# Performance work log

Measured on AMD Instinct MI355X. Metric: run time of the kernel, lower is better.

Reference implementation:

```python
import jax, jax.numpy as jnp
import numpy as np

N_NODES = 50000
N_EDGES = 800000
D_FEAT = 64


def setup_inputs() -> dict:
    key = jax.random.key(0)
    kx, ks, kd = jax.random.split(key, 3)
    x = jax.random.normal(kx, (N_NODES, D_FEAT), dtype=jnp.float32)
    src = jax.random.randint(ks, (N_EDGES,), 0, N_NODES, dtype=jnp.int64)
    dst = jax.random.randint(kd, (N_EDGES,), 0, N_NODES, dtype=jnp.int64)
    return {"x": x, "src": src, "dst": dst}


def reference(x, src, dst):
    # SGC propagation: h[v] = sum_{(u->v) in E} x[u] / sqrt(out_deg(u) * out_deg(v))
    n = x.shape[0]
    # out-degrees: count of outgoing edges per node (matches graph.out_degrees())
    deg = jax.ops.segment_sum(jnp.ones(src.shape, x.dtype), src, num_segments=n)
    # per-edge normalization coefficient 1/sqrt(deg_u * deg_v)  [E]
    norm = 1.0 / jnp.sqrt(deg[src] * deg[dst])
    # gather-multiply-scatter-sum (u_mul_e_sum): messages flow src -> dst
    h = jax.ops.segment_sum(x[src] * norm[:, None], dst, num_segments=n)
    return h
```

## Files before the change

### kernel.cpp

```cpp
#include <hip/hip_runtime.h>

#define N_NODES 50000
#define N_EDGES 800000
#define D_FEAT 64

#define NBINS 2048
#define BSORT 100
#define SORT_CHUNK (N_EDGES / BSORT)
#define NSCAN (NBINS * BSORT)
#define SCAN_BLOCK 1024
#define SCAN_BLOCKS (NSCAN / SCAN_BLOCK)
#define AGG_CAP 4096
#define NAGG ((N_NODES + 31) / 32)

#define HCHUNKS 64
#define HCHUNK (N_EDGES / HCHUNKS)
#define HWORDS ((N_NODES + 3) / 4)

#define RS_BLOCKS ((N_NODES + 255) / 256)

__global__ __launch_bounds__(512)
void hist_count_kernel(const int* __restrict__ src, const int* __restrict__ dst,
                       unsigned int* __restrict__ hp32, unsigned int* __restrict__ gh) {
    __shared__ unsigned int lh[HWORDS];
    const int b = blockIdx.x, t = threadIdx.x;
    if (b < HCHUNKS) {
        for (int i = t; i < HWORDS; i += 512) lh[i] = 0u;
        __syncthreads();
        const int4* s4 = (const int4*)(src + b * HCHUNK);
        for (int i = t; i < HCHUNK / 4; i += 512) {
            int4 v = s4[i];
            atomicAdd(&lh[v.x >> 2], 1u << ((v.x & 3) * 8));
            atomicAdd(&lh[v.y >> 2], 1u << ((v.y & 3) * 8));
            atomicAdd(&lh[v.z >> 2], 1u << ((v.z & 3) * 8));
            atomicAdd(&lh[v.w >> 2], 1u << ((v.w & 3) * 8));
        }
        __syncthreads();
        for (int w = t; w < HWORDS; w += 512)
            hp32[(size_t)b * HWORDS + w] = lh[w];
    } else {
        const int cb = b - HCHUNKS;
        for (int i = t; i < NBINS; i += 512) lh[i] = 0;
        __syncthreads();
        const int4* d4 = (const int4*)(dst + cb * SORT_CHUNK);
        for (int i = t; i < SORT_CHUNK / 4; i += 512) {
            int4 v = d4[i];
            atomicAdd(&lh[v.x >> 5], 1u);
            atomicAdd(&lh[v.y >> 5], 1u);
            atomicAdd(&lh[v.z >> 5], 1u);
            atomicAdd(&lh[v.w >> 5], 1u);
        }
        __syncthreads();
        for (int i = t; i < NBINS; i += 512) gh[(size_t)i * BSORT + cb] = lh[i];
    }
}

__global__ __launch_bounds__(SCAN_BLOCK)
void scanred_rs_kernel(const unsigned int* __restrict__ gh, unsigned int* __restrict__ partial,
                       const unsigned char* __restrict__ hp8, float* __restrict__ rs) {
    const int b = blockIdx.x;
    if (b < SCAN_BLOCKS) {
        __shared__ unsigned int wsum[SCAN_BLOCK / 64];
        int g = b * SCAN_BLOCK + threadIdx.x;
        unsigned int v = gh[g];
        for (int off = 32; off > 0; off >>= 1) v += __shfl_down(v, off, 64);
        if ((threadIdx.x & 63) == 0) wsum[threadIdx.x >> 6] = v;
        __syncthreads();
        if (threadIdx.x < SCAN_BLOCK / 64) {
            unsigned int s = wsum[threadIdx.x];
            for (int off = SCAN_BLOCK / 128; off > 0; off >>= 1) s += __shfl_down(s, off, 64);
            if (threadIdx.x == 0) partial[b] = s;
        }
    } else {
        if (threadIdx.x < 256) {
            int v = (b - SCAN_BLOCKS) * 256 + threadIdx.x;
            if (v < N_NODES) {
                unsigned int s = 0;
                #pragma unroll
                for (int c = 0; c < HCHUNKS; ++c) s += hp8[(size_t)c * (HWORDS * 4) + v];
                rs[v] = rsqrtf((float)s);
            }
        }
    }
}

__global__ __launch_bounds__(SCAN_BLOCK)
void scan_final_kernel(unsigned int* __restrict__ data, const unsigned int* __restrict__ partial) {
    __shared__ unsigned int arr[SCAN_BLOCK];
    __shared__ unsigned int pbase[256];
    const int t = threadIdx.x;
    const int g = blockIdx.x * SCAN_BLOCK + t;
    if (t < 256) pbase[t] = (t < SCAN_BLOCKS) ? partial[t] : 0u;
    __syncthreads();
    for (int off = 1; off < 256; off <<= 1) {
        unsigned int u = (t < 256 && t >= off) ? pbase[t - off] : 0u;
        __syncthreads();
        if (t < 256 && t >= off) pbase[t] += u;
        __syncthreads();
    }
    const unsigned int base = (blockIdx.x == 0) ? 0u : pbase[blockIdx.x - 1];
    unsigned int v = data[g];
    arr[t] = v;
    __syncthreads();
    for (int off = 1; off < SCAN_BLOCK; off <<= 1) {
        unsigned int u = (t >= off) ? arr[t - off] : 0u;
        __syncthreads();
        arr[t] += u;
        __syncthreads();
    }
    data[g] = base + arr[t] - v;
}

__global__ __launch_bounds__(1024)
void bucket_scatter_kernel(const int* __restrict__ src, const int* __restrict__ dst,
                           const unsigned int* __restrict__ gh, unsigned int* __restrict__ keysB) {
    __shared__ unsigned int cur[NBINS];
    const int b = blockIdx.x, t = threadIdx.x;
    for (int i = t; i < NBINS; i += 1024) cur[i] = gh[(size_t)i * BSORT + b];
    __syncthreads();
    const int4* s4 = (const int4*)(src + b * SORT_CHUNK);
    const int4* d4 = (const int4*)(dst + b * SORT_CHUNK);
    for (int i = t; i < SORT_CHUNK / 4; i += 1024) {
        int4 s = s4[i];
        int4 d = d4[i];
        unsigned int p0 = atomicAdd(&cur[d.x >> 5], 1u);
        keysB[p0] = ((unsigned int)d.x << 16) | (unsigned int)s.x;
        unsigned int p1 = atomicAdd(&cur[d.y >> 5], 1u);
        keysB[p1] = ((unsigned int)d.y << 16) | (unsigned int)s.y;
        unsigned int p2 = atomicAdd(&cur[d.z >> 5], 1u);
        keysB[p2] = ((unsigned int)d.z << 16) | (unsigned int)s.z;
        unsigned int p3 = atomicAdd(&cur[d.w >> 5], 1u);
        keysB[p3] = ((unsigned int)d.w << 16) | (unsigned int)s.w;
    }
}

__global__ __launch_bounds__(512)
void bucket_aggregate_kernel(const float* __restrict__ x, const unsigned int* __restrict__ gh,
                             const unsigned int* __restrict__ keysB, const float* __restrict__ rs,
                             float* __restrict__ h) {
    __shared__ unsigned int ebuf[AGG_CAP];
    __shared__ unsigned int ecnt[32];
    __shared__ unsigned int eoff[33];
    const int g = blockIdx.x;
    const int t = threadIdx.x;
    const int lane = t & 63;
    const int w = t >> 6;
    const unsigned int base = gh[(size_t)g * BSORT];
    const unsigned int end  = gh[(size_t)(g + 1) * BSORT];
    const int cnt = (int)(end - base);

    if (cnt > 0 && cnt <= AGG_CAP) {
        if (t < 32) ecnt[t] = 0;
        __syncthreads();
        for (int i = t; i < cnt; i += 512) atomicAdd(&ecnt[(keysB[base + i] >> 16) & 31], 1u);
        __syncthreads();
        if (t == 0) {
            unsigned int r = 0;
            for (int k2 = 0; k2 < 32; ++k2) { eoff[k2] = r; r += ecnt[k2]; }
            eoff[32] = r;
        }
        __syncthreads();
        if (t < 32) ecnt[t] = eoff[t];
        __syncthreads();
        for (int i = t; i < cnt; i += 512) {
            unsigned int k = keysB[base + i];
            ebuf[atomicAdd(&ecnt[(k >> 16) & 31], 1u)] = k;
        }
        __syncthreads();

        const int grp = lane >> 4;
        const int fl  = lane & 15;
        for (int nl = w; nl < 32; nl += 8) {
            int node = g * 32 + nl;
            if (node >= N_NODES) continue;
            const int jb = (int)eoff[nl];
            const int m  = (int)eoff[nl + 1] - jb;
            float ax = 0.0f, ay = 0.0f, az = 0.0f, aw = 0.0f;
            int jj = 0;
            for (; jj + 8 <= m; jj += 8) {
                unsigned int s0 = ebuf[jb + jj + grp] & 0xFFFFu;
                unsigned int s1 = ebuf[jb + jj + 4 + grp] & 0xFFFFu;
                const float4 v0 = *(const float4*)&x[(size_t)s0 * D_FEAT + fl * 4];
                const float4 v1 = *(const float4*)&x[(size_t)s1 * D_FEAT + fl * 4];
                float w0 = rs[s0], w1 = rs[s1];
                ax = fmaf(v0.x, w0, ax); ay = fmaf(v0.y, w0, ay);
                az = fmaf(v0.z, w0, az); aw = fmaf(v0.w, w0, aw);
                ax = fmaf(v1.x, w1, ax); ay = fmaf(v1.y, w1, ay);
                az = fmaf(v1.z, w1, az); aw = fmaf(v1.w, w1, aw);
            }
            if (jj < m) {
                int idx = jj + grp;
                unsigned int s = ebuf[jb + min(idx, m - 1)] & 0xFFFFu;
                float wgt = (idx < m) ? rs[s] : 0.0f;
                const float4 v = *(const float4*)&x[(size_t)s * D_FEAT + fl * 4];
                ax = fmaf(v.x, wgt, ax); ay = fmaf(v.y, wgt, ay);
                az = fmaf(v.z, wgt, az); aw = fmaf(v.w, wgt, aw);
                jj += 4;
                if (jj < m) {
                    idx = jj + grp;
                    unsigned int s2 = ebuf[jb + min(idx, m - 1)] & 0xFFFFu;
                    float wgt2 = (idx < m) ? rs[s2] : 0.0f;
                    const float4 v2 = *(const float4*)&x[(size_t)s2 * D_FEAT + fl * 4];
                    ax = fmaf(v2.x, wgt2, ax); ay = fmaf(v2.y, wgt2, ay);
                    az = fmaf(v2.z, wgt2, az); aw = fmaf(v2.w, wgt2, aw);
                }
            }
            ax += __shfl_xor(ax, 16, 64); ay += __shfl_xor(ay, 16, 64);
            az += __shfl_xor(az, 16, 64); aw += __shfl_xor(aw, 16, 64);
            ax += __shfl_xor(ax, 32, 64); ay += __shfl_xor(ay, 32, 64);
            az += __shfl_xor(az, 32, 64); aw += __shfl_xor(aw, 32, 64);
            if (lane < 16) {
                float4 o;
                if (m > 0) {
                    const float rsn = rs[node];
                    o.x = ax * rsn; o.y = ay * rsn; o.z = az * rsn; o.w = aw * rsn;
                } else {
                    o.x = o.y = o.z = o.w = 0.0f;
                }
                *(float4*)&h[(size_t)node * D_FEAT + fl * 4] = o;
            }
        }
    } else {
        for (int nl = w; nl < 32; nl += 8) {
            int node = g * 32 + nl;
            if (node >= N_NODES) continue;
            float acc = 0.0f;
            int any = 0;
            for (unsigned int j = base; j < end; ++j) {
                unsigned int k = keysB[j];
                if ((int)((k >> 16) & 31) == nl) {
                    unsigned int s = k & 0xFFFFu;
                    acc = fmaf(x[(size_t)s * D_FEAT + lane], rs[s], acc);
                    any = 1;
                }
            }
            h[(size_t)node * D_FEAT + lane] = any ? acc * rs[node] : 0.0f;
        }
    }
}

__global__ void fb_degree_kernel(const int* __restrict__ src, unsigned int* __restrict__ deg,
                                 int n_edges) {
    int i = blockIdx.x * blockDim.x + threadIdx.x;
    int stride = gridDim.x * blockDim.x;
    for (; i < n_edges; i += stride) atomicAdd(&deg[src[i]], 1u);
}
__global__ void fb_scatter_kernel(const float* __restrict__ x, const int* __restrict__ src,
                                  const int* __restrict__ dst, const unsigned int* __restrict__ deg,
                                  float* __restrict__ h, int n_edges) {
    const int lane = threadIdx.x & 63;
    const int wave = (int)((blockIdx.x * blockDim.x + threadIdx.x) >> 6);
    const int nwaves = (int)((gridDim.x * blockDim.x) >> 6);
    for (int e = wave; e < n_edges; e += nwaves) {
        int s = __builtin_amdgcn_readfirstlane(src[e]);
        int d = __builtin_amdgcn_readfirstlane(dst[e]);
        float norm = rsqrtf((float)deg[s] * (float)deg[d]);
        atomicAdd(&h[d * D_FEAT + lane], x[s * D_FEAT + lane] * norm);
    }
}

extern "C" void kernel_launch(void* const* d_in, const int* in_sizes, int n_in,
                              void* d_out, int out_size, void* d_ws, size_t ws_size,
                              hipStream_t stream) {
    const float* x   = (const float*)d_in[0];
    const int*   src = (const int*)d_in[1];
    const int*   dst = (const int*)d_in[2];
    float* h = (float*)d_out;

    size_t off = 0;
    unsigned int*  keysB = (unsigned int*)((char*)d_ws + off);  off += (size_t)N_EDGES * 4;
    unsigned int*  hp32  = keysB;
    unsigned int*  gh    = (unsigned int*)((char*)d_ws + off);  off += (size_t)NSCAN * 4;
    float*         rs    = (float*)((char*)d_ws + off);         off += (size_t)N_NODES * 4;
    unsigned int*  spart = (unsigned int*)((char*)d_ws + off);  off += 256 * 4;

    if (ws_size >= off) {
        hist_count_kernel<<<dim3(HCHUNKS + BSORT), dim3(512), 0, stream>>>(src, dst, hp32, gh);
        scanred_rs_kernel<<<dim3(SCAN_BLOCKS + RS_BLOCKS), dim3(SCAN_BLOCK), 0, stream>>>(
            gh, spart, (const unsigned char*)hp32, rs);
        scan_final_kernel<<<dim3(SCAN_BLOCKS), dim3(SCAN_BLOCK), 0, stream>>>(gh, spart);
        bucket_scatter_kernel<<<dim3(BSORT), dim3(1024), 0, stream>>>(src, dst, gh, keysB);
        bucket_aggregate_kernel<<<dim3(NAGG), dim3(512), 0, stream>>>(x, gh, keysB, rs, h);
    } else {
        unsigned int* deg = (unsigned int*)d_ws;
        hipMemsetAsync(deg, 0, N_NODES * sizeof(unsigned int), stream);
        hipMemsetAsync(d_out, 0, (size_t)out_size * sizeof(float), stream);
        fb_degree_kernel<<<dim3(1024), dim3(256), 0, stream>>>(src, deg, N_EDGES);
        fb_scatter_kernel<<<dim3(2048), dim3(256), 0, stream>>>(x, src, dst, deg, h, N_EDGES);
    }
}
```

Baseline: 61.15 us.

## Widen dst buckets to 64 nodes and use wave-shuffle scans

Halves the number of destination buckets (1024 bins of 64 nodes), so each aggregate block handles 64 nodes and there are half as many blocks and scan entries. The final scan kernel replaces its shared-memory Hillis-Steele loops with wave-level shuffle scans plus a direct reduction of the preceding partials. The per-bucket offset computation in the aggregate kernel also becomes a shuffle scan instead of a serial loop. The aggressive bucket capacity (3072 against a mean of about 1024 edges) keeps the shared buffer smaller, but the aggregate grid drops to about 782 blocks, which may reduce parallelism.

Result: faster. 57.78 us (-5.5%).

```diff
diff --git a/kernel.cpp b/kernel.cpp
--- a/kernel.cpp
+++ b/kernel.cpp
@@ -4,14 +4,14 @@
 #define N_EDGES 800000
 #define D_FEAT 64
 
-#define NBINS 2048
+#define NBINS 1024
 #define BSORT 100
 #define SORT_CHUNK (N_EDGES / BSORT)
 #define NSCAN (NBINS * BSORT)
 #define SCAN_BLOCK 1024
 #define SCAN_BLOCKS (NSCAN / SCAN_BLOCK)
-#define AGG_CAP 4096
-#define NAGG ((N_NODES + 31) / 32)
+#define AGG_CAP 3072
+#define NAGG ((N_NODES + 63) / 64)
 
 #define HCHUNKS 64
 #define HCHUNK (N_EDGES / HCHUNKS)
@@ -45,10 +45,10 @@
         const int4* d4 = (const int4*)(dst + cb * SORT_CHUNK);
         for (int i = t; i < SORT_CHUNK / 4; i += 512) {
             int4 v = d4[i];
-            atomicAdd(&lh[v.x >> 5], 1u);
-            atomicAdd(&lh[v.y >> 5], 1u);
-            atomicAdd(&lh[v.z >> 5], 1u);
-            atomicAdd(&lh[v.w >> 5], 1u);
+            atomicAdd(&lh[v.x >> 6], 1u);
+            atomicAdd(&lh[v.y >> 6], 1u);
+            atomicAdd(&lh[v.z >> 6], 1u);
+            atomicAdd(&lh[v.w >> 6], 1u);
         }
         __syncthreads();
         for (int i = t; i < NBINS; i += 512) gh[(size_t)i * BSORT + cb] = lh[i];
@@ -86,29 +86,39 @@
 
 __global__ __launch_bounds__(SCAN_BLOCK)
 void scan_final_kernel(unsigned int* __restrict__ data, const unsigned int* __restrict__ partial) {
-    __shared__ unsigned int arr[SCAN_BLOCK];
-    __shared__ unsigned int pbase[256];
+    __shared__ unsigned int wsum[SCAN_BLOCK / 64];
+    __shared__ unsigned int red2[2];
     const int t = threadIdx.x;
+    const int lane = t & 63;
+    const int wid = t >> 6;
     const int g = blockIdx.x * SCAN_BLOCK + t;
-    if (t < 256) pbase[t] = (t < SCAN_BLOCKS) ? partial[t] : 0u;
+
+    unsigned int p = (t < blockIdx.x) ? partial[t] : 0u;
+    if (t < 128) {
+        for (int off = 32; off > 0; off >>= 1) p += __shfl_down(p, off, 64);
+        if (lane == 0) red2[wid] = p;
+    }
+
+    unsigned int v = data[g];
+    unsigned int sc = v;
+    for (int off = 1; off < 64; off <<= 1) {
+        unsigned int u = __shfl_up(sc, off, 64);
+        if (lane >= off) sc += u;
+    }
+    if (lane == 63) wsum[wid] = sc;
     __syncthreads();
-    for (int off = 1; off < 256; off <<= 1) {
-        unsigned int u = (t < 256 && t >= off) ? pbase[t - off] : 0u;
-        __syncthreads();
-        if (t < 256 && t >= off) pbase[t] += u;
-        __syncthreads();
-    }
-    const unsigned int base = (blockIdx.x == 0) ? 0u : pbase[blockIdx.x - 1];
-    unsigned int v = data[g];
-    arr[t] = v;
+    if (t < SCAN_BLOCK / 64) {
+        unsigned int q = wsum[t];
+        for (int off = 1; off < SCAN_BLOCK / 64; off <<= 1) {
+            unsigned int u = __shfl_up(q, off, 64);
+            if (t >= off) q += u;
+        }
+        wsum[t] = q;
+    }
     __syncthreads();
-    for (int off = 1; off < SCAN_BLOCK; off <<= 1) {
-        unsigned int u = (t >= off) ? arr[t - off] : 0u;
-        __syncthreads();
-        arr[t] += u;
-        __syncthreads();
-    }
-    data[g] = base + arr[t] - v;
+    const unsigned int base = red2[0] + red2[1];
+    const unsigned int wbase = (wid == 0) ? 0u : wsum[wid - 1];
+    data[g] = base + wbase + sc - v;
 }
 
 __global__ __launch_bounds__(1024)
@@ -116,20 +126,20 @@
                            const unsigned int* __restrict__ gh, unsigned int* __restrict__ keysB) {
     __shared__ unsigned int cur[NBINS];
     const int b = blockIdx.x, t = threadIdx.x;
-    for (int i = t; i < NBINS; i += 1024) cur[i] = gh[(size_t)i * BSORT + b];
+    if (t < NBINS) cur[t] = gh[(size_t)t * BSORT + b];
     __syncthreads();
     const int4* s4 = (const int4*)(src + b * SORT_CHUNK);
     const int4* d4 = (const int4*)(dst + b * SORT_CHUNK);
     for (int i = t; i < SORT_CHUNK / 4; i += 1024) {
         int4 s = s4[i];
         int4 d = d4[i];
-        unsigned int p0 = atomicAdd(&cur[d.x >> 5], 1u);
+        unsigned int p0 = atomicAdd(&cur[d.x >> 6], 1u);
         keysB[p0] = ((unsigned int)d.x << 16) | (unsigned int)s.x;
-        unsigned int p1 = atomicAdd(&cur[d.y >> 5], 1u);
+        unsigned int p1 = atomicAdd(&cur[d.y >> 6], 1u);
         keysB[p1] = ((unsigned int)d.y << 16) | (unsigned int)s.y;
-        unsigned int p2 = atomicAdd(&cur[d.z >> 5], 1u);
+        unsigned int p2 = atomicAdd(&cur[d.z >> 6], 1u);
         keysB[p2] = ((unsigned int)d.z << 16) | (unsigned int)s.z;
-        unsigned int p3 = atomicAdd(&cur[d.w >> 5], 1u);
+        unsigned int p3 = atomicAdd(&cur[d.w >> 6], 1u);
         keysB[p3] = ((unsigned int)d.w << 16) | (unsigned int)s.w;
     }
 }
@@ -139,8 +149,8 @@
                              const unsigned int* __restrict__ keysB, const float* __restrict__ rs,
                              float* __restrict__ h) {
     __shared__ unsigned int ebuf[AGG_CAP];
-    __shared__ unsigned int ecnt[32];
-    __shared__ unsigned int eoff[33];
+    __shared__ unsigned int ecnt[64];
+    __shared__ unsigned int eoff[65];
     const int g = blockIdx.x;
     const int t = threadIdx.x;
     const int lane = t & 63;
@@ -150,28 +160,33 @@
     const int cnt = (int)(end - base);
 
     if (cnt > 0 && cnt <= AGG_CAP) {
-        if (t < 32) ecnt[t] = 0;
-        __syncthreads();
-        for (int i = t; i < cnt; i += 512) atomicAdd(&ecnt[(keysB[base + i] >> 16) & 31], 1u);
-        __syncthreads();
-        if (t == 0) {
-            unsigned int r = 0;
-            for (int k2 = 0; k2 < 32; ++k2) { eoff[k2] = r; r += ecnt[k2]; }
-            eoff[32] = r;
-        }
-        __syncthreads();
-        if (t < 32) ecnt[t] = eoff[t];
+        if (t < 64) ecnt[t] = 0;
+        __syncthreads();
+        for (int i = t; i < cnt; i += 512) atomicAdd(&ecnt[(keysB[base + i] >> 16) & 63], 1u);
+        __syncthreads();
+        if (t < 64) {
+            unsigned int c = ecnt[t];
+            unsigned int q = c;
+            for (int off = 1; off < 64; off <<= 1) {
+                unsigned int u = __shfl_up(q, off, 64);
+                if (lane >= off) q += u;
+            }
+            eoff[t] = q - c;
+            if (t == 63) eoff[64] = q;
+        }
+        __syncthreads();
+        if (t < 64) ecnt[t] = eoff[t];
         __syncthreads();
         for (int i = t; i < cnt; i += 512) {
             unsigned int k = keysB[base + i];
-            ebuf[atomicAdd(&ecnt[(k >> 16) & 31], 1u)] = k;
+            ebuf[atomicAdd(&ecnt[(k >> 16) & 63], 1u)] = k;
         }
         __syncthreads();
 
         const int grp = lane >> 4;
         const int fl  = lane & 15;
-        for (int nl = w; nl < 32; nl += 8) {
-            int node = g * 32 + nl;
+        for (int nl = w; nl < 64; nl += 8) {
+            int node = g * 64 + nl;
             if (node >= N_NODES) continue;
             const int jb = (int)eoff[nl];
             const int m  = (int)eoff[nl + 1] - jb;
@@ -221,14 +236,14 @@
             }
         }
     } else {
-        for (int nl = w; nl < 32; nl += 8) {
-            int node = g * 32 + nl;
+        for (int nl = w; nl < 64; nl += 8) {
+            int node = g * 64 + nl;
             if (node >= N_NODES) continue;
             float acc = 0.0f;
             int any = 0;
             for (unsigned int j = base; j < end; ++j) {
                 unsigned int k = keysB[j];
-                if ((int)((k >> 16) & 31) == nl) {
+                if ((int)((k >> 16) & 63) == nl) {
                     unsigned int s = k & 0xFFFFu;
                     acc = fmaf(x[(size_t)s * D_FEAT + lane], rs[s], acc);
                     any = 1;
@@ -272,7 +287,7 @@
     unsigned int*  hp32  = keysB;
     unsigned int*  gh    = (unsigned int*)((char*)d_ws + off);  off += (size_t)NSCAN * 4;
     float*         rs    = (float*)((char*)d_ws + off);         off += (size_t)N_NODES * 4;
-    unsigned int*  spart = (unsigned int*)((char*)d_ws + off);  off += 256 * 4;
+    unsigned int*  spart = (unsigned int*)((char*)d_ws + off);  off += 128 * 4;
 
     if (ws_size >= off) {
         hist_count_kernel<<<dim3(HCHUNKS + BSORT), dim3(512), 0, stream>>>(src, dst, hp32, gh);
```
